# Kernel tuning notes

Hardware: AMD Instinct MI355X
Metric: run time of the kernel (lower is better)

## Reference

```python
import jax, jax.numpy as jnp
import numpy as np

DIM = 1024
HEADS = 16
HEAD_DIM = DIM // HEADS
EPS = 1e-5  # torch LayerNorm default


def layer_norm(x, w, b):
    mu = jnp.mean(x, axis=-1, keepdims=True)
    var = jnp.mean(jnp.square(x - mu), axis=-1, keepdims=True)
    return (x - mu) * jax.lax.rsqrt(var + EPS) * w + b


def apply_rope(x, pos):
    # x: [B, H, N, D], pos: [N] int32. Standard 1D rotary, split-half style.
    d2 = x.shape[-1] // 2
    inv_freq = 1.0 / (10000.0 ** (jnp.arange(d2, dtype=jnp.float32) / d2))
    ang = pos.astype(jnp.float32)[:, None] * inv_freq[None, :]  # [N, D/2]
    cos, sin = jnp.cos(ang), jnp.sin(ang)
    x1, x2 = x[..., :d2], x[..., d2:]
    return jnp.concatenate([x1 * cos - x2 * sin, x1 * sin + x2 * cos], axis=-1)


def setup_inputs() -> dict:
    key = jax.random.key(0)
    ks = jax.random.split(key, 8)
    B, N, C = 2, 2048, DIM
    s = 1.0 / np.sqrt(C)
    return {
        "x": jax.random.normal(ks[0], (B, N, C), dtype=jnp.float32),
        "qkv_w": jax.random.normal(ks[1], (3 * C, C), dtype=jnp.float32) * s,
        "qn_w": jnp.ones((HEAD_DIM,), jnp.float32),
        "qn_b": jnp.zeros((HEAD_DIM,), jnp.float32),
        "kn_w": jnp.ones((HEAD_DIM,), jnp.float32),
        "kn_b": jnp.zeros((HEAD_DIM,), jnp.float32),
        "proj_w": jax.random.normal(ks[2], (C, C), dtype=jnp.float32) * s,
        "proj_b": jnp.zeros((C,), jnp.float32),
        "pos": jnp.arange(N, dtype=jnp.int32),
    }


def reference(x, qkv_w, qn_w, qn_b, kn_w, kn_b, proj_w, proj_b, pos):
    B, N, C = x.shape
    H, D = HEADS, HEAD_DIM
    scale = D ** -0.5
    qkv = jnp.einsum('bnc,oc->bno', x, qkv_w).reshape(B, N, 3, H, D)
    qkv = jnp.moveaxis(qkv, (2, 3), (0, 2))  # [3, B, H, N, D]
    q, k, v = qkv[0], qkv[1], qkv[2]
    q = layer_norm(q, qn_w, qn_b)
    k = layer_norm(k, kn_w, kn_b)
    q = apply_rope(q, pos)
    k = apply_rope(k, pos)
    attn = jax.nn.softmax(jnp.einsum('bhqd,bhkd->bhqk', q * scale, k), axis=-1)
    out = jnp.einsum('bhqk,bhkd->bhqd', attn, v)  # [B, H, N, D]
    out = out.transpose(0, 2, 1, 3).reshape(B, N, C)
    return jnp.einsum('bnc,oc->bno', out, proj_w) + proj_b
```

## Files before the change

### kernel.cpp

```cpp
#include <hip/hip_runtime.h>
#include <hip/hip_bf16.h>
#include <math.h>
#include <stdint.h>

#define B 2
#define N 2048
#define C 1024
#define H 16
#define D 64
#define LN_EPS 1e-5f

typedef unsigned short u16;
typedef unsigned int u32;
typedef __attribute__((ext_vector_type(8))) short b16x8;
typedef __attribute__((ext_vector_type(4))) float f32x4;

#define MFMA(a, b, c) __builtin_amdgcn_mfma_f32_16x16x32_bf16(a, b, c, 0, 0, 0)

__device__ __forceinline__ u16 f2bf(float x) {
    u32 u = __float_as_uint(x);
    u32 r = u + 0x7fff + ((u >> 16) & 1);
    return (u16)(r >> 16);
}
__device__ __forceinline__ float bf2f(u16 v) {
    return __uint_as_float(((u32)v) << 16);
}
__device__ __forceinline__ void gload_lds16(const void* g, void* l) {
    __builtin_amdgcn_global_load_lds(
        (__attribute__((address_space(1))) void*)(uintptr_t)g,
        (__attribute__((address_space(3))) void*)l, 16, 0, 0);
}
__device__ __forceinline__ float exp2_asm(float x) {
    float r;
    asm("v_exp_f32 %0, %1" : "=v"(r) : "v"(x));
    return r;
}
__device__ __forceinline__ u32 cvtpk_bf16(float lo, float hi) {
    u32 r;
    asm("v_cvt_pk_bf16_f32 %0, %1, %2" : "=v"(r) : "v"(lo), "v"(hi));
    return r;
}

union PW { u32 w[4]; b16x8 v; };

__global__ __launch_bounds__(256) void castk3(
    const float* __restrict__ a, u16* __restrict__ oa, int na4,
    const float* __restrict__ b, u16* __restrict__ ob, int nb4,
    const float* __restrict__ c, u16* __restrict__ oc, int nc4,
    float* __restrict__ ropetab, const int* __restrict__ pos)
{
    int i = blockIdx.x * 256 + threadIdx.x;
    const float* src; u16* dst; int off;
    if (i < na4) { src = a; dst = oa; off = i; }
    else if (i < na4 + nb4) { src = b; dst = ob; off = i - na4; }
    else if (i < na4 + nb4 + nc4) { src = c; dst = oc; off = i - na4 - nb4; }
    else {
        const int idx = i - (na4 + nb4 + nc4);
        if (idx < N * 32) {
            const int nn = idx >> 5, d2 = idx & 31;
            const float invf = exp2_asm((float)d2 * -0.41524101186092029f);
            const float ang = (float)pos[nn] * invf;
            float2 cs;
            cs.x = cosf(ang);
            cs.y = sinf(ang);
            *(float2*)&ropetab[2 * idx] = cs;
        }
        return;
    }
    float4 v = ((const float4*)src)[off];
    ushort4 o;
    o.x = f2bf(v.x); o.y = f2bf(v.y); o.z = f2bf(v.z); o.w = f2bf(v.w);
    ((ushort4*)dst)[off] = o;
}

template <int MODE, int MF, int NF>
__global__ __launch_bounds__(256) void mfma_gemm(
    const u16* __restrict__ A, const u16* __restrict__ W,
    float* __restrict__ outp, const float* __restrict__ bias,
    u16* __restrict__ qkb, u16* __restrict__ vbuf,
    const float* __restrict__ qnw, const float* __restrict__ qnb,
    const float* __restrict__ knw, const float* __restrict__ knb,
    const float* __restrict__ ropetab, int K)
{
    __shared__ u16 As[2][(32 * MF) * 32];
    __shared__ u16 Ws[2][(32 * NF) * 32];
    const int tid = threadIdx.x;
    const int lane = tid & 63, wave = tid >> 6;
    const int g = lane >> 4, c = lane & 15;
    const int wr = wave >> 1, wc = wave & 1;

    const int nwg = gridDim.x * gridDim.y;
    const int p = blockIdx.x + gridDim.x * blockIdx.y;
    const int bidr = (p & 7) * (nwg >> 3) + (p >> 3);
    const int row0 = (bidr / gridDim.x) * (32 * MF);
    const int col0 = (bidr % gridDim.x) * (32 * NF);

    f32x4 acc[MF][NF];
    #pragma unroll
    for (int m = 0; m < MF; ++m)
        #pragma unroll
        for (int n = 0; n < NF; ++n) acc[m][n] = (f32x4){0.f, 0.f, 0.f, 0.f};

    auto stage = [&](int k0, int bi) {
        #pragma unroll
        for (int rep = 0; rep < MF / 2; ++rep) {
            const int idx = rep * 256 + tid;
            const int r_ = idx >> 2, ch = idx & 3;
            gload_lds16(A + (size_t)(row0 + r_) * K + k0 + ch * 8,
                        As[bi] + rep * 2048 + wave * 512);
        }
        #pragma unroll
        for (int rep = 0; rep < NF / 2; ++rep) {
            const int idx = rep * 256 + tid;
            const int r_ = idx >> 2, ch = idx & 3;
            gload_lds16(W + (size_t)(col0 + r_) * K + k0 + ch * 8,
                        Ws[bi] + rep * 2048 + wave * 512);
        }
    };

    stage(0, 0);
    __syncthreads();
    const int nt = K / 32;
    for (int t = 0; t < nt; ++t) {
        const int bi = t & 1;
        if (t + 1 < nt) stage((t + 1) * 32, bi ^ 1);

        b16x8 af[MF], wf[NF];
        #pragma unroll
        for (int m = 0; m < MF; ++m)
            af[m] = *(const b16x8*)&As[bi][(wr * 16 * MF + m * 16 + c) * 32 + g * 8];
        #pragma unroll
        for (int n = 0; n < NF; ++n)
            wf[n] = *(const b16x8*)&Ws[bi][(wc * 16 * NF + n * 16 + c) * 32 + g * 8];
        #pragma unroll
        for (int m = 0; m < MF; ++m)
            #pragma unroll
            for (int n = 0; n < NF; ++n)
                acc[m][n] = MFMA(af[m], wf[n], acc[m][n]);
        __syncthreads();
    }

    if (MODE == 0) {
        const int colbase = col0 + wc * 16 * NF;
        const int which = colbase >> 10;
        const int hh = (colbase >> 6) & (H - 1);
        if (which == 2) {
            #pragma unroll
            for (int m = 0; m < MF; ++m)
                #pragma unroll
                for (int n = 0; n < NF; ++n)
                    #pragma unroll
                    for (int r = 0; r < 4; ++r) {
                        const int row = row0 + wr * 16 * MF + m * 16 + g * 4 + r;
                        const int bb = row >> 11, nn = row & (N - 1);
                        vbuf[(((size_t)(bb * H + hh)) * N + nn) * 64 + n * 16 + c] =
                            f2bf(acc[m][n][r]);
                    }
        } else {
            const float* wv = which ? knw : qnw;
            const float* bv = which ? knb : qnb;
            float wl[4], bl[4];
            #pragma unroll
            for (int n = 0; n < 4; ++n) { wl[n] = wv[n * 16 + c]; bl[n] = bv[n * 16 + c]; }
            const float qs = which ? 1.0f : 0.18033688011112042f;
            u16* dst = qkb + (size_t)which * (B * H * N * D);
            #pragma unroll
            for (int m = 0; m < MF; ++m)
                #pragma unroll
                for (int r = 0; r < 4; ++r) {
                    const float v0 = acc[m][0][r], v1 = acc[m][1][r];
                    const float v2 = acc[m][2][r], v3 = acc[m][3][r];
                    float s = (v0 + v1) + (v2 + v3);
                    s += __shfl_xor(s, 1, 64); s += __shfl_xor(s, 2, 64);
                    s += __shfl_xor(s, 4, 64); s += __shfl_xor(s, 8, 64);
                    const float mu = s * (1.0f / 64.0f);
                    const float d0 = v0 - mu, d1 = v1 - mu;
                    const float d2_ = v2 - mu, d3 = v3 - mu;
                    float s2 = (d0 * d0 + d1 * d1) + (d2_ * d2_ + d3 * d3);
                    s2 += __shfl_xor(s2, 1, 64); s2 += __shfl_xor(s2, 2, 64);
                    s2 += __shfl_xor(s2, 4, 64); s2 += __shfl_xor(s2, 8, 64);
                    const float rstd = rsqrtf(s2 * (1.0f / 64.0f) + LN_EPS);
                    const float y0 = d0 * rstd * wl[0] + bl[0];
                    const float y1 = d1 * rstd * wl[1] + bl[1];
                    const float y2 = d2_ * rstd * wl[2] + bl[2];
                    const float y3 = d3 * rstd * wl[3] + bl[3];
                    const int row = row0 + wr * 16 * MF + m * 16 + g * 4 + r;
                    const int bb = row >> 11, nn = row & (N - 1);
                    const float2 csa = *(const float2*)&ropetab[(size_t)nn * 64 + 2 * c];
                    const float2 csb = *(const float2*)&ropetab[(size_t)nn * 64 + 2 * (16 + c)];
                    const float o0 = (y0 * csa.x - y2 * csa.y) * qs;
                    const float o2 = (y0 * csa.y + y2 * csa.x) * qs;
                    const float o1 = (y1 * csb.x - y3 * csb.y) * qs;
                    const float o3 = (y1 * csb.y + y3 * csb.x) * qs;
                    u16* rp = dst + (((size_t)(bb * H + hh)) * N + nn) * 64;
                    rp[0 * 16 + c] = f2bf(o0);
                    rp[1 * 16 + c] = f2bf(o1);
                    rp[2 * 16 + c] = f2bf(o2);
                    rp[3 * 16 + c] = f2bf(o3);
                }
        }
    } else {
        #pragma unroll
        for (int m = 0; m < MF; ++m)
            #pragma unroll
            for (int n = 0; n < NF; ++n)
                #pragma unroll
                for (int r = 0; r < 4; ++r) {
                    const int row = row0 + wr * 16 * MF + m * 16 + g * 4 + r;
                    const int col = col0 + wc * 16 * NF + n * 16 + c;
                    outp[(size_t)row * C + col] = acc[m][n][r] + bias[col];
                }
    }
}

__global__ __launch_bounds__(512, 2) void attn_kernel(
    const u16* __restrict__ qkb, const u16* __restrict__ vb, u16* __restrict__ aout)
{
    __shared__ u16 Kl[2][2][64 * 64];
    __shared__ u16 Vt[2][2][64 * 64];
    const int tid = threadIdx.x, lane = tid & 63, wave = tid >> 6;
    const int g = lane >> 4, c = lane & 15;
    const int p_ = blockIdx.x;
    const int bid = (p_ & 7) * 64 + (p_ >> 3);
    const int qt = bid & 15, h = (bid >> 4) & 15, b = bid >> 8;
    const size_t headbase = ((size_t)(b * H + h)) * N * D;
    const u16* Qg = qkb + headbase;
    const u16* Kg = qkb + (size_t)(B * H * N * D) + headbase;
    const u16* Vg = vb + headbase;
    const int q0 = qt * 128 + wave * 16;

    b16x8 qf[2];
    #pragma unroll
    for (int ks = 0; ks < 2; ++ks)
        qf[ks] = *(const b16x8*)&Qg[(size_t)(q0 + c) * 64 + ks * 32 + g * 8];

    f32x4 oacc[4];
    #pragma unroll
    for (int nd = 0; nd < 4; ++nd) oacc[nd] = (f32x4){0.f, 0.f, 0.f, 0.f};
    float l_part = 0.f;

    auto stageK = [&](int kt, u16* dstbuf) {
        const int j = tid >> 3, cc2 = tid & 7;
        const int cg = cc2 ^ (j & 7);
        gload_lds16(Kg + (size_t)(kt * 64 + j) * 64 + cg * 8,
                    dstbuf + (size_t)tid * 8);
    };

    const int vjp = (tid & 31) * 2;
    const int vdg = (tid >> 5) & 7;
    const int vddh = tid >> 8;
    const int vchunk16 = 4 * (vjp >> 5) + ((vjp >> 2) & 3);
    const int vpos = 4 * ((vjp >> 4) & 1) + (vjp & 3);
    ushort4 vA4[2], vB4[2];
    auto loadV2 = [&](int pair) {
        #pragma unroll
        for (int t = 0; t < 2; ++t) {
            const int kt = 2 * pair + t;
            vA4[t] = *(const ushort4*)&Vg[(size_t)(kt * 64 + vjp) * 64 + vdg * 8 + vddh * 4];
            vB4[t] = *(const ushort4*)&Vg[(size_t)(kt * 64 + vjp + 1) * 64 + vdg * 8 + vddh * 4];
        }
    };
    auto writeV2 = [&](int bi) {
        #pragma unroll
        for (int t = 0; t < 2; ++t) {
            const u16 a_[4] = {vA4[t].x, vA4[t].y, vA4[t].z, vA4[t].w};
            const u16 b_[4] = {vB4[t].x, vB4[t].y, vB4[t].z, vB4[t].w};
            #pragma unroll
            for (int i = 0; i < 4; ++i) {
                const int dd = vddh * 4 + i;
                const int d = vdg * 8 + dd;
                const u32 pk = (u32)a_[i] | ((u32)b_[i] << 16);
                *(u32*)((char*)Vt[bi][t] + d * 128 + ((vchunk16 ^ dd) << 4) + vpos * 2) = pk;
            }
        }
    };

    auto compute = [&](const char* Kb, const char* Vb) {
        f32x4 s[4];
        #pragma unroll
        for (int jt = 0; jt < 4; ++jt) s[jt] = (f32x4){0.f, 0.f, 0.f, 0.f};
        __builtin_amdgcn_s_setprio(1);
        #pragma unroll
        for (int jt = 0; jt < 4; ++jt)
            #pragma unroll
            for (int ks = 0; ks < 2; ++ks) {
                const int byteoff = (jt * 16 + c) * 128 + ((ks * 64 + g * 16) ^ ((c & 7) << 4));
                const b16x8 kf = *(const b16x8*)(Kb + byteoff);
                s[jt] = MFMA(kf, qf[ks], s[jt]);
            }
        __builtin_amdgcn_s_setprio(0);

        float psj[4];
        #pragma unroll
        for (int jt = 0; jt < 4; ++jt) {
            #pragma unroll
            for (int r = 0; r < 4; ++r) s[jt][r] = exp2_asm(s[jt][r]);
            psj[jt] = (s[jt][0] + s[jt][1]) + (s[jt][2] + s[jt][3]);
        }
        l_part += (psj[0] + psj[1]) + (psj[2] + psj[3]);

        PW pw[2];
        #pragma unroll
        for (int ks = 0; ks < 2; ++ks)
            #pragma unroll
            for (int wd = 0; wd < 4; ++wd)
                pw[ks].w[wd] = cvtpk_bf16(s[2 * ks + (wd >> 1)][2 * (wd & 1)],
                                          s[2 * ks + (wd >> 1)][2 * (wd & 1) + 1]);

        __builtin_amdgcn_s_setprio(1);
        #pragma unroll
        for (int Dg = 0; Dg < 4; ++Dg) {
            #pragma unroll
            for (int kh = 0; kh < 2; ++kh) {
                const b16x8 vf = *(const b16x8*)(Vb + Dg * 2048 + c * 128 +
                                                 (((4 * kh + g) ^ (c & 7)) << 4));
                oacc[Dg] = MFMA(vf, pw[kh].v, oacc[Dg]);
            }
        }
        __builtin_amdgcn_s_setprio(0);
    };

    loadV2(0);
    stageK(0, (u16*)Kl[0][0]);
    stageK(1, (u16*)Kl[0][1]);
    writeV2(0);
    __syncthreads();

    const int npair = N / 128;
    for (int p = 0; p < npair - 1; ++p) {
        const int bi = p & 1;
        loadV2(p + 1);
        stageK(2 * p + 2, (u16*)Kl[bi ^ 1][0]);
        stageK(2 * p + 3, (u16*)Kl[bi ^ 1][1]);
        compute((const char*)Kl[bi][0], (const char*)Vt[bi][0]);
        compute((const char*)Kl[bi][1], (const char*)Vt[bi][1]);
        writeV2(bi ^ 1);
        __syncthreads();
    }
    {
        const int bi = (npair - 1) & 1;
        compute((const char*)Kl[bi][0], (const char*)Vt[bi][0]);
        compute((const char*)Kl[bi][1], (const char*)Vt[bi][1]);
    }

    float l = l_part;
    l += __shfl_xor(l, 16, 64);
    l += __shfl_xor(l, 32, 64);
    const float li = 1.0f / l;
    #pragma unroll
    for (int Dg = 0; Dg < 4; ++Dg) {
        uint2 pr;
        pr.x = cvtpk_bf16(oacc[Dg][0] * li, oacc[Dg][1] * li);
        pr.y = cvtpk_bf16(oacc[Dg][2] * li, oacc[Dg][3] * li);
        *(uint2*)&aout[((size_t)(b * N + q0 + c)) * C + h * 64 + Dg * 16 + g * 4] = pr;
    }
}

extern "C" void kernel_launch(void* const* d_in, const int* in_sizes, int n_in,
                              void* d_out, int out_size, void* d_ws, size_t ws_size,
                              hipStream_t stream) {
    const float* x      = (const float*)d_in[0];
    const float* qkv_w  = (const float*)d_in[1];
    const float* qn_w   = (const float*)d_in[2];
    const float* qn_b   = (const float*)d_in[3];
    const float* kn_w   = (const float*)d_in[4];
    const float* kn_b   = (const float*)d_in[5];
    const float* proj_w = (const float*)d_in[6];
    const float* proj_b = (const float*)d_in[7];
    const int*   pos    = (const int*)d_in[8];
    float* out = (float*)d_out;

    u16* xb      = (u16*)d_ws;
    u16* wqkvb   = xb + 4194304;
    u16* wprojb  = wqkvb + 3145728;
    u16* qkb     = wprojb + 1048576;
    u16* vbuf    = qkb + 8388608;
    u16* aob     = vbuf + 4194304;
    float* rtab  = (float*)(aob + 4194304);

    castk3<<<8448, 256, 0, stream>>>(x, xb, 1048576,
                                     qkv_w, wqkvb, 786432,
                                     proj_w, wprojb, 262144,
                                     rtab, pos);

    mfma_gemm<0, 2, 4><<<dim3(24, 64), 256, 0, stream>>>(
        xb, wqkvb, nullptr, nullptr, qkb, vbuf,
        qn_w, qn_b, kn_w, kn_b, rtab, C);
    attn_kernel<<<512, 512, 0, stream>>>(qkb, vbuf, aob);
    mfma_gemm<1, 2, 2><<<dim3(16, 64), 256, 0, stream>>>(
        aob, wprojb, out, proj_b, nullptr, nullptr,
        nullptr, nullptr, nullptr, nullptr, nullptr, C);
}
```

Measured before the change: 129.4 us.

## Split attention waves into query-pair by head-dim-half tiles to reuse LDS fragments

```diff
diff --git a/kernel.cpp b/kernel.cpp
--- a/kernel.cpp
+++ b/kernel.cpp
@@ -227,17 +227,22 @@
     const u16* Qg = qkb + headbase;
     const u16* Kg = qkb + (size_t)(B * H * N * D) + headbase;
     const u16* Vg = vb + headbase;
-    const int q0 = qt * 128 + wave * 16;
-
-    b16x8 qf[2];
+    const int qg = wave >> 1, dh = wave & 1;
+    const int q0 = qt * 128 + qg * 32;
+
+    b16x8 qf[2][2];
     #pragma unroll
-    for (int ks = 0; ks < 2; ++ks)
-        qf[ks] = *(const b16x8*)&Qg[(size_t)(q0 + c) * 64 + ks * 32 + g * 8];
-
-    f32x4 oacc[4];
+    for (int qb_ = 0; qb_ < 2; ++qb_)
+        #pragma unroll
+        for (int ks = 0; ks < 2; ++ks)
+            qf[qb_][ks] = *(const b16x8*)&Qg[(size_t)(q0 + qb_ * 16 + c) * 64 + ks * 32 + g * 8];
+
+    f32x4 oacc[2][2];
     #pragma unroll
-    for (int nd = 0; nd < 4; ++nd) oacc[nd] = (f32x4){0.f, 0.f, 0.f, 0.f};
-    float l_part = 0.f;
+    for (int qb_ = 0; qb_ < 2; ++qb_)
+        #pragma unroll
+        for (int n = 0; n < 2; ++n) oacc[qb_][n] = (f32x4){0.f, 0.f, 0.f, 0.f};
+    float l_part[2] = {0.f, 0.f};
 
     auto stageK = [&](int kt, u16* dstbuf) {
         const int j = tid >> 3, cc2 = tid & 7;
@@ -276,9 +281,12 @@
     };
 
     auto compute = [&](const char* Kb, const char* Vb) {
-        f32x4 s[4];
-        #pragma unroll
-        for (int jt = 0; jt < 4; ++jt) s[jt] = (f32x4){0.f, 0.f, 0.f, 0.f};
+        f32x4 s0[4], s1[4];
+        #pragma unroll
+        for (int jt = 0; jt < 4; ++jt) {
+            s0[jt] = (f32x4){0.f, 0.f, 0.f, 0.f};
+            s1[jt] = (f32x4){0.f, 0.f, 0.f, 0.f};
+        }
         __builtin_amdgcn_s_setprio(1);
         #pragma unroll
         for (int jt = 0; jt < 4; ++jt)
@@ -286,35 +294,55 @@
             for (int ks = 0; ks < 2; ++ks) {
                 const int byteoff = (jt * 16 + c) * 128 + ((ks * 64 + g * 16) ^ ((c & 7) << 4));
                 const b16x8 kf = *(const b16x8*)(Kb + byteoff);
-                s[jt] = MFMA(kf, qf[ks], s[jt]);
+                s0[jt] = MFMA(kf, qf[0][ks], s0[jt]);
+                s1[jt] = MFMA(kf, qf[1][ks], s1[jt]);
             }
         __builtin_amdgcn_s_setprio(0);
 
-        float psj[4];
-        #pragma unroll
-        for (int jt = 0; jt < 4; ++jt) {
-            #pragma unroll
-            for (int r = 0; r < 4; ++r) s[jt][r] = exp2_asm(s[jt][r]);
-            psj[jt] = (s[jt][0] + s[jt][1]) + (s[jt][2] + s[jt][3]);
-        }
-        l_part += (psj[0] + psj[1]) + (psj[2] + psj[3]);
-
-        PW pw[2];
-        #pragma unroll
-        for (int ks = 0; ks < 2; ++ks)
-            #pragma unroll
-            for (int wd = 0; wd < 4; ++wd)
-                pw[ks].w[wd] = cvtpk_bf16(s[2 * ks + (wd >> 1)][2 * (wd & 1)],
-                                          s[2 * ks + (wd >> 1)][2 * (wd & 1) + 1]);
+        PW pw0[2], pw1[2];
+        {
+            float psj[4];
+            #pragma unroll
+            for (int jt = 0; jt < 4; ++jt) {
+                #pragma unroll
+                for (int r = 0; r < 4; ++r) s0[jt][r] = exp2_asm(s0[jt][r]);
+                psj[jt] = (s0[jt][0] + s0[jt][1]) + (s0[jt][2] + s0[jt][3]);
+            }
+            l_part[0] += (psj[0] + psj[1]) + (psj[2] + psj[3]);
+            #pragma unroll
+            for (int ks = 0; ks < 2; ++ks)
+                #pragma unroll
+                for (int wd = 0; wd < 4; ++wd)
+                    pw0[ks].w[wd] = cvtpk_bf16(s0[2 * ks + (wd >> 1)][2 * (wd & 1)],
+                                               s0[2 * ks + (wd >> 1)][2 * (wd & 1) + 1]);
+        }
+        {
+            float psj[4];
+            #pragma unroll
+            for (int jt = 0; jt < 4; ++jt) {
+                #pragma unroll
+                for (int r = 0; r < 4; ++r) s1[jt][r] = exp2_asm(s1[jt][r]);
+                psj[jt] = (s1[jt][0] + s1[jt][1]) + (s1[jt][2] + s1[jt][3]);
+            }
+            l_part[1] += (psj[0] + psj[1]) + (psj[2] + psj[3]);
+            #pragma unroll
+            for (int ks = 0; ks < 2; ++ks)
+                #pragma unroll
+                for (int wd = 0; wd < 4; ++wd)
+                    pw1[ks].w[wd] = cvtpk_bf16(s1[2 * ks + (wd >> 1)][2 * (wd & 1)],
+                                               s1[2 * ks + (wd >> 1)][2 * (wd & 1) + 1]);
+        }
 
         __builtin_amdgcn_s_setprio(1);
         #pragma unroll
-        for (int Dg = 0; Dg < 4; ++Dg) {
+        for (int DgL = 0; DgL < 2; ++DgL) {
+            const int Dg = 2 * dh + DgL;
             #pragma unroll
             for (int kh = 0; kh < 2; ++kh) {
                 const b16x8 vf = *(const b16x8*)(Vb + Dg * 2048 + c * 128 +
                                                  (((4 * kh + g) ^ (c & 7)) << 4));
-                oacc[Dg] = MFMA(vf, pw[kh].v, oacc[Dg]);
+                oacc[0][DgL] = MFMA(vf, pw0[kh].v, oacc[0][DgL]);
+                oacc[1][DgL] = MFMA(vf, pw1[kh].v, oacc[1][DgL]);
             }
         }
         __builtin_amdgcn_s_setprio(0);
@@ -343,16 +371,21 @@
         compute((const char*)Kl[bi][1], (const char*)Vt[bi][1]);
     }
 
-    float l = l_part;
-    l += __shfl_xor(l, 16, 64);
-    l += __shfl_xor(l, 32, 64);
-    const float li = 1.0f / l;
     #pragma unroll
-    for (int Dg = 0; Dg < 4; ++Dg) {
-        uint2 pr;
-        pr.x = cvtpk_bf16(oacc[Dg][0] * li, oacc[Dg][1] * li);
-        pr.y = cvtpk_bf16(oacc[Dg][2] * li, oacc[Dg][3] * li);
-        *(uint2*)&aout[((size_t)(b * N + q0 + c)) * C + h * 64 + Dg * 16 + g * 4] = pr;
+    for (int qb_ = 0; qb_ < 2; ++qb_) {
+        float l = l_part[qb_];
+        l += __shfl_xor(l, 16, 64);
+        l += __shfl_xor(l, 32, 64);
+        const float li = 1.0f / l;
+        #pragma unroll
+        for (int DgL = 0; DgL < 2; ++DgL) {
+            const int Dg = 2 * dh + DgL;
+            uint2 pr;
+            pr.x = cvtpk_bf16(oacc[qb_][DgL][0] * li, oacc[qb_][DgL][1] * li);
+            pr.y = cvtpk_bf16(oacc[qb_][DgL][2] * li, oacc[qb_][DgL][3] * li);
+            *(uint2*)&aout[((size_t)(b * N + q0 + qb_ * 16 + c)) * C +
+                           h * 64 + Dg * 16 + g * 4] = pr;
+        }
     }
 }
 
```

Result: slower. 167.1 us (+29.2%).
